# Performance work log

Hardware: AMD Instinct MI355X
Metric: run time of the kernel (lower is better)

Reference implementation:

```python
import jax, jax.numpy as jnp
import numpy as np

N = 131072   # total inner-graph nodes (G * n)
G = 2048     # number of inner graphs = nodes of outer graph fg
n = 64       # nodes per inner graph (contiguous blocks)
E = 1048576  # inner edges
EF = 32768   # outer (fg) edges
D = 128      # emb_dim == hidden_dim
K = 8        # SortPooling k
VOCAB = 150


def setup_inputs() -> dict:
    key = jax.random.key(0)
    ks = jax.random.split(key, 32)
    p = lambda k, shape: (jax.random.normal(k, shape, jnp.float32) * 0.1)
    inp = {
        'h': jax.random.randint(ks[0], (N,), 0, VOCAB),
        'g_src': jax.random.randint(ks[1], (E,), 0, N),
        'g_dst': jax.random.randint(ks[2], (E,), 0, N),
        'fg_src': jax.random.randint(ks[3], (EF,), 0, G),
        'fg_dst': jax.random.randint(ks[4], (EF,), 0, G),
        'token_emb': p(ks[5], (VOCAB, D)),
        # GATConv 1 (D -> D, 1 head): fc weight (in,out), attn vectors, output bias
        'W1': p(ks[6], (D, D)), 'al1': p(ks[7], (D,)), 'ar1': p(ks[8], (D,)), 'b1': p(ks[9], (D,)),
        # GATConv 2
        'W2': p(ks[10], (D, D)), 'al2': p(ks[11], (D,)), 'ar2': p(ks[12], (D,)), 'b2': p(ks[13], (D,)),
        # GATConv 3 (K*D -> D) over fg
        'W3': p(ks[14], (K * D, D)), 'al3': p(ks[15], (D,)), 'ar3': p(ks[16], (D,)), 'b3': p(ks[17], (D,)),
        # linear_forward
        'Wf': p(ks[18], (D, D)), 'bf': p(ks[19], (D,)),
        # linear
        'Wl': p(ks[20], (D, D)), 'bl': p(ks[21], (D,)),
        # linear1
        'Wl1': p(ks[22], (D, D)), 'bl1': p(ks[23], (D,)),
        # clasifier
        'Wc': p(ks[24], (D, 2)), 'bc': p(ks[25], (2,)),
    }
    return inp


def gat_conv(src, dst, num_nodes, x, W, al, ar, b):
    """DGL GATConv, num_heads=1, allow_zero_in_degree=True, no activation."""
    f = x @ W                                   # [N, D] projected features
    el = f @ al                                 # [N] left attention logits
    er = f @ ar                                 # [N] right attention logits
    e = jax.nn.leaky_relu(el[src] + er[dst], 0.2)   # [E] per-edge score
    m = jax.ops.segment_max(e, dst, num_segments=num_nodes)
    a = jnp.exp(e - m[dst])
    s = jax.ops.segment_sum(a, dst, num_segments=num_nodes)
    alpha = a / s[dst]                          # edge softmax over incoming edges
    out = jax.ops.segment_sum(alpha[:, None] * f[src], dst, num_segments=num_nodes)
    return out + b                              # zero-in-degree nodes -> bias only


def sort_pooling(x, num_graphs, nodes_per_graph, k):
    """DGL SortPooling: sort each node's feature ascending, rank nodes by last
    channel descending, take top-k, concat -> [G, k*D]."""
    d = x.shape[-1]
    x = jnp.sort(x.reshape(num_graphs, nodes_per_graph, d), axis=-1)
    idx = jnp.argsort(-x[:, :, -1], axis=1)[:, :k]          # [G, k]
    topk = jnp.take_along_axis(x, idx[:, :, None], axis=1)  # [G, k, D]
    return topk.reshape(num_graphs, k * d)


def reference(h, g_src, g_dst, fg_src, fg_dst, token_emb,
              W1, al1, ar1, b1, W2, al2, ar2, b2, W3, al3, ar3, b3,
              Wf, bf, Wl, bl, Wl1, bl1, Wc, bc):
    x = jax.nn.relu(token_emb[h])                                   # [N, D]
    x = jax.nn.relu(gat_conv(g_src, g_dst, N, x, W1, al1, ar1, b1))
    x = jax.nn.relu(gat_conv(g_src, g_dst, N, x, W2, al2, ar2, b2))
    x = jax.nn.relu(x @ Wf + bf)                                    # linear_forward
    x = sort_pooling(x, G, n, K)                                    # [G, K*D]
    x = jax.nn.relu(gat_conv(fg_src, fg_dst, G, x, W3, al3, ar3, b3))
    x = jax.nn.relu(x @ Wl + bl)                                    # dropout = eval identity
    x = jax.nn.relu(x @ Wl1 + bl1)
    x = x @ Wc + bc
    return x.reshape(-1, 2)
```

## Files before the change

kernel.cpp:

```cpp
#include <hip/hip_runtime.h>
#include <math.h>

#define NN   131072
#define GG   2048
#define NPG  64
#define EE   1048576
#define EFN  32768
#define DD   128
#define KK   8

typedef unsigned short bfu;
typedef short bf16x8 __attribute__((ext_vector_type(8)));
typedef float f32x4 __attribute__((ext_vector_type(4)));

static __device__ __forceinline__ bfu f2b(float f) {
  unsigned u = __float_as_uint(f);
  u += 0x7FFFu + ((u >> 16) & 1u);
  return (bfu)(u >> 16);
}
static __device__ __forceinline__ float b2f(bfu b) {
  return __uint_as_float(((unsigned)b) << 16);
}

__global__ void fill_f32_kernel(float* __restrict__ p, float v, int nElems) {
  int i = blockIdx.x * 256 + threadIdx.x;
  if (i < nElems) p[i] = v;
}

__global__ void zero_int_kernel(int* __restrict__ p, int nElems) {
  int i = blockIdx.x * 256 + threadIdx.x;
  if (i < nElems) p[i] = 0;
}

__global__ void init_softmax_kernel(float* __restrict__ mx, float* __restrict__ sm, int nElems) {
  int i = blockIdx.x * 256 + threadIdx.x;
  if (i < nElems) { mx[i] = -INFINITY; sm[i] = 0.f; }
}

__global__ void embed_relu_kernel(const float* __restrict__ temb,
                                  const int* __restrict__ h,
                                  float* __restrict__ x, int total) {
  int i = blockIdx.x * 256 + threadIdx.x;
  if (i >= total) return;
  int node = i >> 7, d = i & 127;
  x[i] = fmaxf(temb[h[node] * DD + d], 0.f);
}

template <int KD, int ROWS>
__global__ __launch_bounds__(128) void gemm_kernel(
    const float* __restrict__ A, const float* __restrict__ W,
    const float* __restrict__ bias, float* __restrict__ out,
    int relu_flag) {
  __shared__ float As[ROWS * KD];
  const int row0 = blockIdx.x * ROWS;
  const int tid = threadIdx.x;
  for (int i = tid; i < ROWS * KD; i += 128) As[i] = A[(size_t)row0 * KD + i];
  __syncthreads();
  float acc[ROWS];
#pragma unroll
  for (int r = 0; r < ROWS; r++) acc[r] = 0.f;
  for (int k = 0; k < KD; k++) {
    float w = W[k * 128 + tid];
#pragma unroll
    for (int r = 0; r < ROWS; r++) acc[r] += As[r * KD + k] * w;
  }
  float b = bias ? bias[tid] : 0.f;
#pragma unroll
  for (int r = 0; r < ROWS; r++) {
    float v = acc[r] + b;
    if (relu_flag) v = fmaxf(v, 0.f);
    out[(size_t)(row0 + r) * 128 + tid] = v;
  }
}

__global__ __launch_bounds__(256) void gemm1024_kernel(
    const float* __restrict__ A, const float* __restrict__ W,
    float* __restrict__ out) {
  __shared__ float As[8 * 1024];
  __shared__ float red[8][256];
  const int t = threadIdx.x;
  const int row0 = blockIdx.x * 8;
  for (int idx = t; idx < 8 * 256; idx += 256) {
    int r = idx >> 8, c4 = (idx & 255) << 2;
    *(float4*)&As[r * 1024 + c4] = *(const float4*)(A + (size_t)(row0 + r) * 1024 + c4);
  }
  __syncthreads();
  const int col = t & 127, kh = t >> 7;
  const int k0 = kh * 512;
  float acc[8];
#pragma unroll
  for (int r = 0; r < 8; r++) acc[r] = 0.f;
  for (int k = k0; k < k0 + 512; k += 4) {
    float w0 = W[(size_t)(k + 0) * 128 + col];
    float w1 = W[(size_t)(k + 1) * 128 + col];
    float w2 = W[(size_t)(k + 2) * 128 + col];
    float w3 = W[(size_t)(k + 3) * 128 + col];
#pragma unroll
    for (int r = 0; r < 8; r++) {
      float4 a = *(const float4*)&As[r * 1024 + k];
      acc[r] += a.x * w0 + a.y * w1 + a.z * w2 + a.w * w3;
    }
  }
#pragma unroll
  for (int r = 0; r < 8; r++) red[r][t] = acc[r];
  __syncthreads();
  for (int idx = t; idx < 1024; idx += 256) {
    int r = idx >> 7, c = idx & 127;
    out[(size_t)(row0 + r) * 128 + c] = red[r][c] + red[r][128 + c];
  }
}

__global__ void pack_w_kernel(const float* __restrict__ W,
                              bfu* __restrict__ hi, bfu* __restrict__ lo) {
  int i = blockIdx.x * 256 + threadIdx.x;
  if (i >= 16384) return;
  int k = i >> 7, n = i & 127;
  float w = W[i];
  bfu h = f2b(w);
  bfu l = f2b(w - b2f(h));
  int kk = k >> 5, k5 = k & 31, quad = k5 >> 3, j = k5 & 7;
  int tt = n >> 4, m16 = n & 15;
  int pos = ((((kk * 8 + tt) * 4 + quad) * 16) + m16) * 8 + j;
  hi[pos] = h;
  lo[pos] = l;
}

template <int SRC_MODE, int EPI>
__global__ __launch_bounds__(256) void mfma_gemm(
    const float* A, const float* __restrict__ temb,
    const int* __restrict__ hidx,
    const bfu* __restrict__ WfHi, const bfu* __restrict__ WfLo,
    const float* __restrict__ bias, void* out,
    const float* __restrict__ al, const float* __restrict__ ar,
    float* __restrict__ el, float* __restrict__ er,
    float* __restrict__ keyb) {
  const int t = threadIdx.x;
  const int lane = t & 63, wv_ = t >> 6;
  const int m16 = lane & 15, quad = lane >> 4;
  const int rowbase = blockIdx.x * 128 + wv_ * 32;
  const float* arow0 = (SRC_MODE == 1) ? (temb + (size_t)hidx[rowbase + m16] * 128)
                                       : (A + (size_t)(rowbase + m16) * 128);
  const float* arow1 = (SRC_MODE == 1) ? (temb + (size_t)hidx[rowbase + 16 + m16] * 128)
                                       : (A + (size_t)(rowbase + 16 + m16) * 128);
  f32x4 acc[2][8];
#pragma unroll
  for (int rg = 0; rg < 2; rg++)
#pragma unroll
    for (int i = 0; i < 8; i++) acc[rg][i] = (f32x4){0.f, 0.f, 0.f, 0.f};
#pragma unroll
  for (int kk = 0; kk < 4; kk++) {
    int k0 = kk * 32 + quad * 8;
    float av0[8], av1[8];
    *(float4*)&av0[0] = *(const float4*)(arow0 + k0);
    *(float4*)&av0[4] = *(const float4*)(arow0 + k0 + 4);
    *(float4*)&av1[0] = *(const float4*)(arow1 + k0);
    *(float4*)&av1[4] = *(const float4*)(arow1 + k0 + 4);
    if (SRC_MODE == 1) {
#pragma unroll
      for (int i = 0; i < 8; i++) {
        av0[i] = fmaxf(av0[i], 0.f);
        av1[i] = fmaxf(av1[i], 0.f);
      }
    }
    bf16x8 ahi0, alo0, ahi1, alo1;
#pragma unroll
    for (int i = 0; i < 8; i++) {
      bfu h0 = f2b(av0[i]);
      alo0[i] = (short)f2b(av0[i] - b2f(h0));
      ahi0[i] = (short)h0;
      bfu h1 = f2b(av1[i]);
      alo1[i] = (short)f2b(av1[i] - b2f(h1));
      ahi1[i] = (short)h1;
    }
#pragma unroll
    for (int tt = 0; tt < 8; tt++) {
      int pos = ((((kk * 8 + tt) * 4 + quad) * 16) + m16) * 8;
      bf16x8 bhi = *(const bf16x8*)&WfHi[pos];
      bf16x8 blo = *(const bf16x8*)&WfLo[pos];
      acc[0][tt] = __builtin_amdgcn_mfma_f32_16x16x32_bf16(ahi0, bhi, acc[0][tt], 0, 0, 0);
      acc[0][tt] = __builtin_amdgcn_mfma_f32_16x16x32_bf16(ahi0, blo, acc[0][tt], 0, 0, 0);
      acc[0][tt] = __builtin_amdgcn_mfma_f32_16x16x32_bf16(alo0, bhi, acc[0][tt], 0, 0, 0);
      acc[1][tt] = __builtin_amdgcn_mfma_f32_16x16x32_bf16(ahi1, bhi, acc[1][tt], 0, 0, 0);
      acc[1][tt] = __builtin_amdgcn_mfma_f32_16x16x32_bf16(ahi1, blo, acc[1][tt], 0, 0, 0);
      acc[1][tt] = __builtin_amdgcn_mfma_f32_16x16x32_bf16(alo1, bhi, acc[1][tt], 0, 0, 0);
    }
  }
#pragma unroll
  for (int rg = 0; rg < 2; rg++) {
    const int rb = rowbase + rg * 16;
    if (EPI == 1) {
      float pl[4] = {0.f, 0.f, 0.f, 0.f}, pr[4] = {0.f, 0.f, 0.f, 0.f};
#pragma unroll
      for (int tt = 0; tt < 8; tt++) {
        int col = tt * 16 + m16;
        float alv = al[col], arv = ar[col];
#pragma unroll
        for (int r = 0; r < 4; r++) {
          float v = acc[rg][tt][r];
          ((bfu*)out)[(size_t)(rb + quad * 4 + r) * 128 + col] = f2b(v);
          pl[r] += v * alv;
          pr[r] += v * arv;
        }
      }
#pragma unroll
      for (int r = 0; r < 4; r++) {
        float a0 = pl[r], a1 = pr[r];
#pragma unroll
        for (int off = 1; off < 16; off <<= 1) {
          a0 += __shfl_xor(a0, off);
          a1 += __shfl_xor(a1, off);
        }
        if (m16 == 0) {
          el[rb + quad * 4 + r] = a0;
          er[rb + quad * 4 + r] = a1;
        }
      }
    } else {
      float pm[4] = {-INFINITY, -INFINITY, -INFINITY, -INFINITY};
#pragma unroll
      for (int tt = 0; tt < 8; tt++) {
        int col = tt * 16 + m16;
        float bv = bias[col];
#pragma unroll
        for (int r = 0; r < 4; r++) {
          float v = fmaxf(acc[rg][tt][r] + bv, 0.f);
          ((float*)out)[(size_t)(rb + quad * 4 + r) * 128 + col] = v;
          pm[r] = fmaxf(pm[r], v);
        }
      }
#pragma unroll
      for (int r = 0; r < 4; r++) {
        float a0 = pm[r];
#pragma unroll
        for (int off = 1; off < 16; off <<= 1) a0 = fmaxf(a0, __shfl_xor(a0, off));
        if (m16 == 0) keyb[rb + quad * 4 + r] = a0;
      }
    }
  }
}

__global__ __launch_bounds__(64) void attn_logits_kernel(
    const float* __restrict__ f, const float* __restrict__ al,
    const float* __restrict__ ar, float* __restrict__ el,
    float* __restrict__ er) {
  int node = blockIdx.x, lane = threadIdx.x;
  float v1 = f[(size_t)node * 128 + lane];
  float v2 = f[(size_t)node * 128 + 64 + lane];
  float sl = v1 * al[lane] + v2 * al[64 + lane];
  float sr = v1 * ar[lane] + v2 * ar[64 + lane];
#pragma unroll
  for (int off = 32; off; off >>= 1) {
    sl += __shfl_down(sl, off);
    sr += __shfl_down(sr, off);
  }
  if (lane == 0) { el[node] = sl; er[node] = sr; }
}

__global__ void hist_rank_kernel(const int* __restrict__ dst, int* __restrict__ cnt,
                                 int* __restrict__ rank, int nE) {
  int e = blockIdx.x * 256 + threadIdx.x;
  if (e < nE) rank[e] = atomicAdd(&cnt[dst[e]], 1);
}

__global__ __launch_bounds__(256) void scan_block_kernel(
    const int* __restrict__ cnt, int* __restrict__ excl, int* __restrict__ part) {
  __shared__ int s[256];
  int blk = blockIdx.x, tid = threadIdx.x;
  int base = blk * 1024 + tid * 4;
  int a0 = cnt[base], a1 = cnt[base + 1], a2 = cnt[base + 2], a3 = cnt[base + 3];
  int tsum = a0 + a1 + a2 + a3;
  s[tid] = tsum; __syncthreads();
  for (int off = 1; off < 256; off <<= 1) {
    int v = (tid >= off) ? s[tid - off] : 0;
    __syncthreads();
    s[tid] += v;
    __syncthreads();
  }
  int texcl = s[tid] - tsum;
  excl[base]     = texcl;
  excl[base + 1] = texcl + a0;
  excl[base + 2] = texcl + a0 + a1;
  excl[base + 3] = texcl + a0 + a1 + a2;
  if (tid == 255) part[blk] = s[255];
}

__global__ __launch_bounds__(128) void scan_part_kernel(int* __restrict__ part) {
  __shared__ int s[128];
  int tid = threadIdx.x;
  int orig = part[tid];
  s[tid] = orig; __syncthreads();
  for (int off = 1; off < 128; off <<= 1) {
    int v = (tid >= off) ? s[tid - off] : 0;
    __syncthreads();
    s[tid] += v;
    __syncthreads();
  }
  part[tid] = s[tid] - orig;
}

__global__ void scan_add_kernel(int* __restrict__ row_ptr, const int* __restrict__ part,
                                int n, int total) {
  int i = blockIdx.x * 256 + threadIdx.x;
  if (i < n) row_ptr[i] += part[i >> 10];
  if (i == 0) row_ptr[n] = total;
}

__global__ __launch_bounds__(256) void scan2048_kernel(const int* __restrict__ cnt,
                                                       int* __restrict__ rp, int total) {
  __shared__ int s[256];
  int t = threadIdx.x;
  int base = t * 8;
  int v[8];
  int tsum = 0;
#pragma unroll
  for (int i = 0; i < 8; i++) { v[i] = cnt[base + i]; tsum += v[i]; }
  s[t] = tsum; __syncthreads();
  for (int off = 1; off < 256; off <<= 1) {
    int x = (t >= off) ? s[t - off] : 0;
    __syncthreads();
    s[t] += x;
    __syncthreads();
  }
  int excl = s[t] - tsum;
#pragma unroll
  for (int i = 0; i < 8; i++) { rp[base + i] = excl; excl += v[i]; }
  if (t == 255) rp[2048] = total;
}

__global__ void scatter2_kernel(const int* __restrict__ dst, const int* __restrict__ src,
                                const int* __restrict__ row_ptr, const int* __restrict__ rank,
                                int* __restrict__ adj_src, int nE) {
  int e = blockIdx.x * 256 + threadIdx.x;
  if (e >= nE) return;
  adj_src[row_ptr[dst[e]] + rank[e]] = src[e];
}

__global__ __launch_bounds__(256) void gat_aggregate_csr_kernel(
    const bfu* __restrict__ F, const float* __restrict__ el,
    const float* __restrict__ er, const int* __restrict__ row_ptr,
    const int* __restrict__ adj_src,
    const float* __restrict__ bias, float* __restrict__ outX) {
  const int t = threadIdx.x;
  const int l = t & 31;
  const int gb = t & 32;
  const int d = blockIdx.x * 8 + (t >> 5);
  const int c0 = l * 4;
  int beg = row_ptr[d];
  int n = row_ptr[d + 1] - beg;
  float4 bv = *(const float4*)&bias[c0];
  if (n == 0) {
    float4 o;
    o.x = fmaxf(bv.x, 0.f); o.y = fmaxf(bv.y, 0.f);
    o.z = fmaxf(bv.z, 0.f); o.w = fmaxf(bv.w, 0.f);
    *(float4*)&outX[(size_t)d * 128 + c0] = o;
    return;
  }
  float er_d = er[d];
  float4 acc = make_float4(0.f, 0.f, 0.f, 0.f);
  if (n <= 32) {
    int sv = 0; float sc = -INFINITY;
    if (l < n) {
      sv = adj_src[beg + l];
      float v = el[sv] + er_d;
      sc = v > 0.f ? v : 0.2f * v;
    }
    float m = sc;
#pragma unroll
    for (int off = 16; off; off >>= 1) m = fmaxf(m, __shfl_xor(m, off));
    float ex = (l < n) ? expf(sc - m) : 0.f;
    float s = ex;
#pragma unroll
    for (int off = 16; off; off >>= 1) s += __shfl_xor(s, off);
    float wt = ex / s;
    for (int j = 0; j < n; j += 4) {
      int   s0 = __shfl(sv, gb + j);
      float w0 = __shfl(wt, gb + j);
      int   j1 = (j + 1 < n) ? j + 1 : j;
      int   s1 = __shfl(sv, gb + j1); float w1 = (j + 1 < n) ? __shfl(wt, gb + j1) : 0.f;
      int   j2 = (j + 2 < n) ? j + 2 : j;
      int   s2 = __shfl(sv, gb + j2); float w2 = (j + 2 < n) ? __shfl(wt, gb + j2) : 0.f;
      int   j3 = (j + 3 < n) ? j + 3 : j;
      int   s3 = __shfl(sv, gb + j3); float w3 = (j + 3 < n) ? __shfl(wt, gb + j3) : 0.f;
      ushort4 f0 = *(const ushort4*)&F[(size_t)s0 * 128 + c0];
      ushort4 f1 = *(const ushort4*)&F[(size_t)s1 * 128 + c0];
      ushort4 f2 = *(const ushort4*)&F[(size_t)s2 * 128 + c0];
      ushort4 f3 = *(const ushort4*)&F[(size_t)s3 * 128 + c0];
      acc.x += w0 * b2f(f0.x) + w1 * b2f(f1.x) + w2 * b2f(f2.x) + w3 * b2f(f3.x);
      acc.y += w0 * b2f(f0.y) + w1 * b2f(f1.y) + w2 * b2f(f2.y) + w3 * b2f(f3.y);
      acc.z += w0 * b2f(f0.z) + w1 * b2f(f1.z) + w2 * b2f(f2.z) + w3 * b2f(f3.z);
      acc.w += w0 * b2f(f0.w) + w1 * b2f(f1.w) + w2 * b2f(f2.w) + w3 * b2f(f3.w);
    }
  } else {
    float lm = -INFINITY;
    for (int e = l; e < n; e += 32) {
      int sv = adj_src[beg + e];
      float v = el[sv] + er_d;
      v = v > 0.f ? v : 0.2f * v;
      lm = fmaxf(lm, v);
    }
#pragma unroll
    for (int off = 16; off; off >>= 1) lm = fmaxf(lm, __shfl_xor(lm, off));
    float ls = 0.f;
    for (int e = l; e < n; e += 32) {
      int sv = adj_src[beg + e];
      float v = el[sv] + er_d;
      v = v > 0.f ? v : 0.2f * v;
      ls += expf(v - lm);
    }
#pragma unroll
    for (int off = 16; off; off >>= 1) ls += __shfl_xor(ls, off);
    for (int base = 0; base < n; base += 32) {
      int e = base + l;
      int sv = 0; float wt = 0.f;
      if (e < n) {
        sv = adj_src[beg + e];
        float v = el[sv] + er_d;
        v = v > 0.f ? v : 0.2f * v;
        wt = expf(v - lm) / ls;
      }
      int cnt = min(32, n - base);
      for (int j = 0; j < cnt; ++j) {
        int s0 = __shfl(sv, gb + j);
        float w0 = __shfl(wt, gb + j);
        ushort4 f0 = *(const ushort4*)&F[(size_t)s0 * 128 + c0];
        acc.x += w0 * b2f(f0.x);
        acc.y += w0 * b2f(f0.y);
        acc.z += w0 * b2f(f0.z);
        acc.w += w0 * b2f(f0.w);
      }
    }
  }
  float4 o;
  o.x = fmaxf(acc.x + bv.x, 0.f);
  o.y = fmaxf(acc.y + bv.y, 0.f);
  o.z = fmaxf(acc.z + bv.z, 0.f);
  o.w = fmaxf(acc.w + bv.w, 0.f);
  *(float4*)&outX[(size_t)d * 128 + c0] = o;
}

__global__ __launch_bounds__(256) void gat_aggregate_outer_kernel(
    const float* __restrict__ F, const float* __restrict__ el,
    const float* __restrict__ er, const int* __restrict__ row_ptr,
    const int* __restrict__ adj_src,
    const float* __restrict__ bias, float* __restrict__ outG) {
  const int t = threadIdx.x;
  const int l = t & 31;
  const int gb = t & 32;
  const int d = blockIdx.x * 8 + (t >> 5);
  const int c0 = l * 4;
  int beg = row_ptr[d];
  int n = row_ptr[d + 1] - beg;
  float4 bv = *(const float4*)&bias[c0];
  if (n == 0) {
    float4 o;
    o.x = fmaxf(bv.x, 0.f); o.y = fmaxf(bv.y, 0.f);
    o.z = fmaxf(bv.z, 0.f); o.w = fmaxf(bv.w, 0.f);
    *(float4*)&outG[(size_t)d * 128 + c0] = o;
    return;
  }
  float er_d = er[d];
  float4 acc = make_float4(0.f, 0.f, 0.f, 0.f);
  if (n <= 32) {
    int sv = 0; float sc = -INFINITY;
    if (l < n) {
      sv = adj_src[beg + l];
      float v = el[sv] + er_d;
      sc = v > 0.f ? v : 0.2f * v;
    }
    float m = sc;
#pragma unroll
    for (int off = 16; off; off >>= 1) m = fmaxf(m, __shfl_xor(m, off));
    float ex = (l < n) ? expf(sc - m) : 0.f;
    float s = ex;
#pragma unroll
    for (int off = 16; off; off >>= 1) s += __shfl_xor(s, off);
    float wt = ex / s;
    for (int j = 0; j < n; ++j) {
      int   s0 = __shfl(sv, gb + j);
      float w0 = __shfl(wt, gb + j);
      float4 f0 = *(const float4*)&F[(size_t)s0 * 128 + c0];
      acc.x += w0 * f0.x; acc.y += w0 * f0.y;
      acc.z += w0 * f0.z; acc.w += w0 * f0.w;
    }
  } else {
    float lm = -INFINITY;
    for (int e = l; e < n; e += 32) {
      int sv = adj_src[beg + e];
      float v = el[sv] + er_d;
      v = v > 0.f ? v : 0.2f * v;
      lm = fmaxf(lm, v);
    }
#pragma unroll
    for (int off = 16; off; off >>= 1) lm = fmaxf(lm, __shfl_xor(lm, off));
    float ls = 0.f;
    for (int e = l; e < n; e += 32) {
      int sv = adj_src[beg + e];
      float v = el[sv] + er_d;
      v = v > 0.f ? v : 0.2f * v;
      ls += expf(v - lm);
    }
#pragma unroll
    for (int off = 16; off; off >>= 1) ls += __shfl_xor(ls, off);
    for (int base = 0; base < n; base += 32) {
      int e = base + l;
      int sv = 0; float wt = 0.f;
      if (e < n) {
        sv = adj_src[beg + e];
        float v = el[sv] + er_d;
        v = v > 0.f ? v : 0.2f * v;
        wt = expf(v - lm) / ls;
      }
      int cnt = min(32, n - base);
      for (int j = 0; j < cnt; ++j) {
        int s0 = __shfl(sv, gb + j);
        float w0 = __shfl(wt, gb + j);
        float4 f0 = *(const float4*)&F[(size_t)s0 * 128 + c0];
        acc.x += w0 * f0.x; acc.y += w0 * f0.y;
        acc.z += w0 * f0.z; acc.w += w0 * f0.w;
      }
    }
  }
  float4 o;
  o.x = fmaxf(acc.x + bv.x, 0.f);
  o.y = fmaxf(acc.y + bv.y, 0.f);
  o.z = fmaxf(acc.z + bv.z, 0.f);
  o.w = fmaxf(acc.w + bv.w, 0.f);
  *(float4*)&outG[(size_t)d * 128 + c0] = o;
}

static __device__ __forceinline__ void atomicMaxF(float* addr, float v) {
  int iv = __float_as_int(v);
  if (iv >= 0) atomicMax((int*)addr, iv);
  else atomicMin((unsigned int*)addr, (unsigned int)iv);
}

static __device__ __forceinline__ float edge_score(const float* el, const float* er,
                                                   int sv, int dv) {
  float v = el[sv] + er[dv];
  return v > 0.f ? v : 0.2f * v;
}

__global__ void edge_max_kernel(const float* __restrict__ el,
                                const float* __restrict__ er,
                                const int* __restrict__ src,
                                const int* __restrict__ dst,
                                float* __restrict__ m, int nE) {
  int e = blockIdx.x * 256 + threadIdx.x;
  if (e >= nE) return;
  atomicMaxF(&m[dst[e]], edge_score(el, er, src[e], dst[e]));
}

__global__ void edge_expsum_kernel(const float* __restrict__ el,
                                   const float* __restrict__ er,
                                   const float* __restrict__ m,
                                   const int* __restrict__ src,
                                   const int* __restrict__ dst,
                                   float* __restrict__ s, int nE) {
  int e = blockIdx.x * 256 + threadIdx.x;
  if (e >= nE) return;
  int d = dst[e];
  atomicAdd(&s[d], expf(edge_score(el, er, src[e], d) - m[d]));
}

__global__ __launch_bounds__(128) void edge_aggregate_kernel(
    const float* __restrict__ f, const float* __restrict__ el,
    const float* __restrict__ er, const float* __restrict__ m,
    const float* __restrict__ s, const int* __restrict__ src,
    const int* __restrict__ dst, float* __restrict__ out, int nE) {
  int e = blockIdx.x;
  int d = threadIdx.x;
  int sv = src[e], dv = dst[e];
  float alpha = expf(edge_score(el, er, sv, dv) - m[dv]) / s[dv];
  atomicAdd(&out[(size_t)dv * 128 + d], alpha * f[(size_t)sv * 128 + d]);
}

__global__ void bias_relu_kernel(float* __restrict__ x,
                                 const float* __restrict__ b, int total) {
  int i = blockIdx.x * 256 + threadIdx.x;
  if (i >= total) return;
  x[i] = fmaxf(x[i] + b[i & 127], 0.f);
}

__global__ __launch_bounds__(64) void row_max_kernel(const float* __restrict__ x,
                                                     float* __restrict__ key) {
  int node = blockIdx.x, lane = threadIdx.x;
  float v = fmaxf(x[(size_t)node * 128 + lane], x[(size_t)node * 128 + 64 + lane]);
#pragma unroll
  for (int off = 32; off; off >>= 1) v = fmaxf(v, __shfl_down(v, off));
  if (lane == 0) key[node] = v;
}

__global__ __launch_bounds__(64) void select_topk_kernel(
    const float* __restrict__ key, int* __restrict__ sel) {
  __shared__ float keys[NPG];
  int g = blockIdx.x, t = threadIdx.x;
  keys[t] = key[(size_t)g * NPG + t];
  __syncthreads();
  float myk = keys[t];
  int rank = 0;
  for (int j = 0; j < NPG; ++j) {
    float kj = keys[j];
    rank += (kj > myk) || (kj == myk && j < t);
  }
  if (rank < KK) sel[g * KK + rank] = t;
}

__global__ __launch_bounds__(128) void sort_rows_kernel(
    const float* __restrict__ x, const int* __restrict__ sel,
    float* __restrict__ xp) {
  __shared__ float v[128];
  int b = blockIdx.x;
  int t = threadIdx.x;
  int g = b >> 3, r = b & 7;
  int node = sel[b];
  v[t] = x[(size_t)(g * NPG + node) * 128 + t];
  __syncthreads();
  for (int k = 2; k <= 128; k <<= 1) {
    for (int j = k >> 1; j > 0; j >>= 1) {
      int ixj = t ^ j;
      if (ixj > t) {
        float a = v[t], bb = v[ixj];
        bool asc = ((t & k) == 0);
        if (asc ? (a > bb) : (a < bb)) { v[t] = bb; v[ixj] = a; }
      }
      __syncthreads();
    }
  }
  xp[(size_t)g * (KK * 128) + r * 128 + t] = v[t];
}

__global__ __launch_bounds__(128) void mlp_tail_kernel(
    const float* __restrict__ g3, const float* __restrict__ Wl,
    const float* __restrict__ bl, const float* __restrict__ Wl1,
    const float* __restrict__ bl1, const float* __restrict__ Wc,
    const float* __restrict__ bc, float* __restrict__ out) {
  __shared__ float buf[128];
  __shared__ float r0[128], r1[128];
  int g = blockIdx.x, t = threadIdx.x;
  buf[t] = g3[(size_t)g * 128 + t];
  __syncthreads();
  float a = 0.f;
  for (int k = 0; k < 128; k++) a += buf[k] * Wl[k * 128 + t];
  float t1 = fmaxf(a + bl[t], 0.f);
  __syncthreads();
  buf[t] = t1;
  __syncthreads();
  a = 0.f;
  for (int k = 0; k < 128; k++) a += buf[k] * Wl1[k * 128 + t];
  float t2 = fmaxf(a + bl1[t], 0.f);
  r0[t] = t2 * Wc[t * 2 + 0];
  r1[t] = t2 * Wc[t * 2 + 1];
  __syncthreads();
  for (int off = 64; off; off >>= 1) {
    if (t < off) { r0[t] += r0[t + off]; r1[t] += r1[t + off]; }
    __syncthreads();
  }
  if (t == 0) {
    out[g * 2 + 0] = r0[0] + bc[0];
    out[g * 2 + 1] = r1[0] + bc[1];
  }
}

extern "C" void kernel_launch(void* const* d_in, const int* in_sizes, int n_in,
                              void* d_out, int out_size, void* d_ws, size_t ws_size,
                              hipStream_t stream) {
  const size_t BASE_FLOATS = (size_t)NN * DD * 2 + (size_t)NN * 4;
  const size_t CSR_INTS = (size_t)(NN + 1) + NN + EE + 128;
  if (ws_size < BASE_FLOATS * sizeof(float)) {
    hipMemsetAsync(d_out, 0, (size_t)out_size * sizeof(float), stream);
    return;
  }
  const bool use_csr = ws_size >= BASE_FLOATS * sizeof(float) + CSR_INTS * sizeof(int);

  const int* h      = (const int*)d_in[0];
  const int* g_src  = (const int*)d_in[1];
  const int* g_dst  = (const int*)d_in[2];
  const int* fg_src = (const int*)d_in[3];
  const int* fg_dst = (const int*)d_in[4];
  const float* temb = (const float*)d_in[5];
  const float* W1 = (const float*)d_in[6];
  const float* al1 = (const float*)d_in[7];
  const float* ar1 = (const float*)d_in[8];
  const float* b1 = (const float*)d_in[9];
  const float* W2 = (const float*)d_in[10];
  const float* al2 = (const float*)d_in[11];
  const float* ar2 = (const float*)d_in[12];
  const float* b2 = (const float*)d_in[13];
  const float* W3 = (const float*)d_in[14];
  const float* al3 = (const float*)d_in[15];
  const float* ar3 = (const float*)d_in[16];
  const float* b3 = (const float*)d_in[17];
  const float* Wf = (const float*)d_in[18];
  const float* bfv = (const float*)d_in[19];
  const float* Wl = (const float*)d_in[20];
  const float* bl = (const float*)d_in[21];
  const float* Wl1 = (const float*)d_in[22];
  const float* bl1 = (const float*)d_in[23];
  const float* Wc = (const float*)d_in[24];
  const float* bc = (const float*)d_in[25];
  float* out = (float*)d_out;

  float* ws = (float*)d_ws;
  float* X  = ws;
  float* F  = X + (size_t)NN * DD;
  float* el = F + (size_t)NN * DD;
  float* er = el + NN;
  float* mx = er + NN;
  float* sm = mx + NN;
  int* row_ptr = (int*)(sm + NN);
  int* cursor  = row_ptr + NN + 1;
  int* adj_src = cursor + NN;
  int* part    = adj_src + EE;
  int* rankb = (int*)X;
  bfu* w1h = (bfu*)mx;
  bfu* w1l = w1h + 16384;
  bfu* w2h = w1l + 16384;
  bfu* w2l = w2h + 16384;
  bfu* wfh = w2l + 16384;
  bfu* wfl = wfh + 16384;
  int* ocnt  = (int*)X;
  int* orp   = ocnt + 2048;
  int* orank = orp + 2080;
  int* oadj  = orank + EFN;
  float* xp   = F;
  float* f3   = F + 2097152;
  float* g3   = f3 + (size_t)GG * DD;
  float* t1   = g3 + (size_t)GG * DD;
  float* t2   = t1 + (size_t)GG * DD;
  float* keyb = t2 + (size_t)GG * DD;
  int*   sel  = (int*)(keyb + NN);

  const int totalND = NN * DD;

  if (use_csr) {
    bfu* Fb = (bfu*)F;
    zero_int_kernel<<<NN / 256, 256, 0, stream>>>(cursor, NN);
    hist_rank_kernel<<<EE / 256, 256, 0, stream>>>(g_dst, cursor, rankb, EE);
    scan_block_kernel<<<NN / 1024, 256, 0, stream>>>(cursor, row_ptr, part);
    scan_part_kernel<<<1, 128, 0, stream>>>(part);
    scan_add_kernel<<<(NN + 255) / 256, 256, 0, stream>>>(row_ptr, part, NN, EE);
    scatter2_kernel<<<EE / 256, 256, 0, stream>>>(g_dst, g_src, row_ptr, rankb, adj_src, EE);

    pack_w_kernel<<<64, 256, 0, stream>>>(W1, w1h, w1l);
    pack_w_kernel<<<64, 256, 0, stream>>>(W2, w2h, w2l);
    pack_w_kernel<<<64, 256, 0, stream>>>(Wf, wfh, wfl);

    mfma_gemm<1, 1><<<NN / 128, 256, 0, stream>>>(
        nullptr, temb, h, w1h, w1l, nullptr, Fb, al1, ar1, el, er, nullptr);
    gat_aggregate_csr_kernel<<<NN / 8, 256, 0, stream>>>(Fb, el, er, row_ptr, adj_src, b1, X);

    mfma_gemm<0, 1><<<NN / 128, 256, 0, stream>>>(
        X, nullptr, nullptr, w2h, w2l, nullptr, Fb, al2, ar2, el, er, nullptr);
    gat_aggregate_csr_kernel<<<NN / 8, 256, 0, stream>>>(Fb, el, er, row_ptr, adj_src, b2, X);

    mfma_gemm<0, 2><<<NN / 128, 256, 0, stream>>>(
        X, nullptr, nullptr, wfh, wfl, bfv, X, nullptr, nullptr, nullptr, nullptr, keyb);

    select_topk_kernel<<<GG, 64, 0, stream>>>(keyb, sel);
    sort_rows_kernel<<<GG * KK, 128, 0, stream>>>(X, sel, xp);

    gemm1024_kernel<<<GG / 8, 256, 0, stream>>>(xp, W3, f3);
    attn_logits_kernel<<<GG, 64, 0, stream>>>(f3, al3, ar3, el, er);
    zero_int_kernel<<<GG / 256, 256, 0, stream>>>(ocnt, GG);
    hist_rank_kernel<<<EFN / 256, 256, 0, stream>>>(fg_dst, ocnt, orank, EFN);
    scan2048_kernel<<<1, 256, 0, stream>>>(ocnt, orp, EFN);
    scatter2_kernel<<<EFN / 256, 256, 0, stream>>>(fg_dst, fg_src, orp, orank, oadj, EFN);
    gat_aggregate_outer_kernel<<<GG / 8, 256, 0, stream>>>(f3, el, er, orp, oadj, b3, g3);

    mlp_tail_kernel<<<GG, 128, 0, stream>>>(g3, Wl, bl, Wl1, bl1, Wc, bc, out);
  } else {
    embed_relu_kernel<<<totalND / 256, 256, 0, stream>>>(temb, h, X, totalND);
    auto gat_inner = [&](const float* W, const float* al, const float* ar, const float* bb) {
      gemm_kernel<DD, 8><<<NN / 8, 128, 0, stream>>>(X, W, nullptr, F, 0);
      attn_logits_kernel<<<NN, 64, 0, stream>>>(F, al, ar, el, er);
      init_softmax_kernel<<<(NN + 255) / 256, 256, 0, stream>>>(mx, sm, NN);
      fill_f32_kernel<<<totalND / 256, 256, 0, stream>>>(X, 0.f, totalND);
      edge_max_kernel<<<(EE + 255) / 256, 256, 0, stream>>>(el, er, g_src, g_dst, mx, EE);
      edge_expsum_kernel<<<(EE + 255) / 256, 256, 0, stream>>>(el, er, mx, g_src, g_dst, sm, EE);
      edge_aggregate_kernel<<<EE, 128, 0, stream>>>(F, el, er, mx, sm, g_src, g_dst, X, EE);
      bias_relu_kernel<<<totalND / 256, 256, 0, stream>>>(X, bb, totalND);
    };
    gat_inner(W1, al1, ar1, b1);
    gat_inner(W2, al2, ar2, b2);
    gemm_kernel<DD, 8><<<NN / 8, 128, 0, stream>>>(X, Wf, bfv, X, 1);
    row_max_kernel<<<NN, 64, 0, stream>>>(X, keyb);

    select_topk_kernel<<<GG, 64, 0, stream>>>(keyb, sel);
    sort_rows_kernel<<<GG * KK, 128, 0, stream>>>(X, sel, xp);

    gemm1024_kernel<<<GG / 8, 256, 0, stream>>>(xp, W3, f3);
    attn_logits_kernel<<<GG, 64, 0, stream>>>(f3, al3, ar3, el, er);
    init_softmax_kernel<<<(GG + 255) / 256, 256, 0, stream>>>(mx, sm, GG);
    fill_f32_kernel<<<(GG * DD + 255) / 256, 256, 0, stream>>>(g3, 0.f, GG * DD);
    edge_max_kernel<<<(EFN + 255) / 256, 256, 0, stream>>>(el, er, fg_src, fg_dst, mx, EFN);
    edge_expsum_kernel<<<(EFN + 255) / 256, 256, 0, stream>>>(el, er, mx, fg_src, fg_dst, sm, EFN);
    edge_aggregate_kernel<<<EFN, 128, 0, stream>>>(f3, el, er, mx, sm, fg_src, fg_dst, g3, EFN);
    bias_relu_kernel<<<(GG * DD + 255) / 256, 256, 0, stream>>>(g3, b3, GG * DD);
    mlp_tail_kernel<<<GG, 128, 0, stream>>>(g3, Wl, bl, Wl1, bl1, Wc, bc, out);
  }
}
```

Before: 473.6 us.

## Switch inner GAT activations and MFMA split to fp16, store X as half

Replaces the bf16 hi/lo split with an fp16 hi/lo split for weights and projected features. Aggregation outputs and the linear_forward output are now stored as fp16 instead of fp32, halving activation traffic. The two subsequent GEMMs read them directly through a new source mode, skipping the A-lo correction MFMA and the fp32-to-split conversion. The risk is fp16 range and precision loss on activations, plus a changed numeric path feeding sort pooling's ranking and ties.

```diff
diff --git a/kernel.cpp b/kernel.cpp
--- a/kernel.cpp
+++ b/kernel.cpp
@@ -10,7 +10,7 @@
 #define KK   8
 
 typedef unsigned short bfu;
-typedef short bf16x8 __attribute__((ext_vector_type(8)));
+typedef _Float16 f16x8 __attribute__((ext_vector_type(8)));
 typedef float f32x4 __attribute__((ext_vector_type(4)));
 
 static __device__ __forceinline__ bfu f2b(float f) {
@@ -20,6 +20,18 @@
 }
 static __device__ __forceinline__ float b2f(bfu b) {
   return __uint_as_float(((unsigned)b) << 16);
+}
+
+static __device__ __forceinline__ bfu f2h(float f) {
+  _Float16 h = (_Float16)f;
+  bfu u;
+  __builtin_memcpy(&u, &h, 2);
+  return u;
+}
+static __device__ __forceinline__ float h2f(bfu b) {
+  _Float16 h;
+  __builtin_memcpy(&h, &b, 2);
+  return (float)h;
 }
 
 __global__ void fill_f32_kernel(float* __restrict__ p, float v, int nElems) {
@@ -116,8 +128,8 @@
   if (i >= 16384) return;
   int k = i >> 7, n = i & 127;
   float w = W[i];
-  bfu h = f2b(w);
-  bfu l = f2b(w - b2f(h));
+  bfu h = f2h(w);
+  bfu l = f2h(w - h2f(h));
   int kk = k >> 5, k5 = k & 31, quad = k5 >> 3, j = k5 & 7;
   int tt = n >> 4, m16 = n & 15;
   int pos = ((((kk * 8 + tt) * 4 + quad) * 16) + m16) * 8 + j;
@@ -138,10 +150,20 @@
   const int lane = t & 63, wv_ = t >> 6;
   const int m16 = lane & 15, quad = lane >> 4;
   const int rowbase = blockIdx.x * 128 + wv_ * 32;
-  const float* arow0 = (SRC_MODE == 1) ? (temb + (size_t)hidx[rowbase + m16] * 128)
-                                       : (A + (size_t)(rowbase + m16) * 128);
-  const float* arow1 = (SRC_MODE == 1) ? (temb + (size_t)hidx[rowbase + 16 + m16] * 128)
-                                       : (A + (size_t)(rowbase + 16 + m16) * 128);
+  const float* arow0 = nullptr;
+  const float* arow1 = nullptr;
+  const bfu* brow0 = nullptr;
+  const bfu* brow1 = nullptr;
+  if constexpr (SRC_MODE == 1) {
+    arow0 = temb + (size_t)hidx[rowbase + m16] * 128;
+    arow1 = temb + (size_t)hidx[rowbase + 16 + m16] * 128;
+  } else if constexpr (SRC_MODE == 0) {
+    arow0 = A + (size_t)(rowbase + m16) * 128;
+    arow1 = A + (size_t)(rowbase + 16 + m16) * 128;
+  } else {
+    brow0 = (const bfu*)A + (size_t)(rowbase + m16) * 128;
+    brow1 = (const bfu*)A + (size_t)(rowbase + 16 + m16) * 128;
+  }
   f32x4 acc[2][8];
 #pragma unroll
   for (int rg = 0; rg < 2; rg++)
@@ -150,45 +172,52 @@
 #pragma unroll
   for (int kk = 0; kk < 4; kk++) {
     int k0 = kk * 32 + quad * 8;
-    float av0[8], av1[8];
-    *(float4*)&av0[0] = *(const float4*)(arow0 + k0);
-    *(float4*)&av0[4] = *(const float4*)(arow0 + k0 + 4);
-    *(float4*)&av1[0] = *(const float4*)(arow1 + k0);
-    *(float4*)&av1[4] = *(const float4*)(arow1 + k0 + 4);
-    if (SRC_MODE == 1) {
+    f16x8 ahi0, alo0, ahi1, alo1;
+    if constexpr (SRC_MODE == 2) {
+      ahi0 = *(const f16x8*)(brow0 + k0);
+      ahi1 = *(const f16x8*)(brow1 + k0);
+    } else {
+      float av0[8], av1[8];
+      *(float4*)&av0[0] = *(const float4*)(arow0 + k0);
+      *(float4*)&av0[4] = *(const float4*)(arow0 + k0 + 4);
+      *(float4*)&av1[0] = *(const float4*)(arow1 + k0);
+      *(float4*)&av1[4] = *(const float4*)(arow1 + k0 + 4);
+      if (SRC_MODE == 1) {
+#pragma unroll
+        for (int i = 0; i < 8; i++) {
+          av0[i] = fmaxf(av0[i], 0.f);
+          av1[i] = fmaxf(av1[i], 0.f);
+        }
+      }
 #pragma unroll
       for (int i = 0; i < 8; i++) {
-        av0[i] = fmaxf(av0[i], 0.f);
-        av1[i] = fmaxf(av1[i], 0.f);
-      }
-    }
-    bf16x8 ahi0, alo0, ahi1, alo1;
-#pragma unroll
-    for (int i = 0; i < 8; i++) {
-      bfu h0 = f2b(av0[i]);
-      alo0[i] = (short)f2b(av0[i] - b2f(h0));
-      ahi0[i] = (short)h0;
-      bfu h1 = f2b(av1[i]);
-      alo1[i] = (short)f2b(av1[i] - b2f(h1));
-      ahi1[i] = (short)h1;
+        _Float16 h0 = (_Float16)av0[i];
+        ahi0[i] = h0;
+        alo0[i] = (_Float16)(av0[i] - (float)h0);
+        _Float16 h1 = (_Float16)av1[i];
+        ahi1[i] = h1;
+        alo1[i] = (_Float16)(av1[i] - (float)h1);
+      }
     }
 #pragma unroll
     for (int tt = 0; tt < 8; tt++) {
       int pos = ((((kk * 8 + tt) * 4 + quad) * 16) + m16) * 8;
-      bf16x8 bhi = *(const bf16x8*)&WfHi[pos];
-      bf16x8 blo = *(const bf16x8*)&WfLo[pos];
-      acc[0][tt] = __builtin_amdgcn_mfma_f32_16x16x32_bf16(ahi0, bhi, acc[0][tt], 0, 0, 0);
-      acc[0][tt] = __builtin_amdgcn_mfma_f32_16x16x32_bf16(ahi0, blo, acc[0][tt], 0, 0, 0);
-      acc[0][tt] = __builtin_amdgcn_mfma_f32_16x16x32_bf16(alo0, bhi, acc[0][tt], 0, 0, 0);
-      acc[1][tt] = __builtin_amdgcn_mfma_f32_16x16x32_bf16(ahi1, bhi, acc[1][tt], 0, 0, 0);
-      acc[1][tt] = __builtin_amdgcn_mfma_f32_16x16x32_bf16(ahi1, blo, acc[1][tt], 0, 0, 0);
-      acc[1][tt] = __builtin_amdgcn_mfma_f32_16x16x32_bf16(alo1, bhi, acc[1][tt], 0, 0, 0);
+      f16x8 bhi = *(const f16x8*)&WfHi[pos];
+      f16x8 blo = *(const f16x8*)&WfLo[pos];
+      acc[0][tt] = __builtin_amdgcn_mfma_f32_16x16x32_f16(ahi0, bhi, acc[0][tt], 0, 0, 0);
+      acc[0][tt] = __builtin_amdgcn_mfma_f32_16x16x32_f16(ahi0, blo, acc[0][tt], 0, 0, 0);
+      if constexpr (SRC_MODE != 2)
+        acc[0][tt] = __builtin_amdgcn_mfma_f32_16x16x32_f16(alo0, bhi, acc[0][tt], 0, 0, 0);
+      acc[1][tt] = __builtin_amdgcn_mfma_f32_16x16x32_f16(ahi1, bhi, acc[1][tt], 0, 0, 0);
+      acc[1][tt] = __builtin_amdgcn_mfma_f32_16x16x32_f16(ahi1, blo, acc[1][tt], 0, 0, 0);
+      if constexpr (SRC_MODE != 2)
+        acc[1][tt] = __builtin_amdgcn_mfma_f32_16x16x32_f16(alo1, bhi, acc[1][tt], 0, 0, 0);
     }
   }
 #pragma unroll
   for (int rg = 0; rg < 2; rg++) {
     const int rb = rowbase + rg * 16;
-    if (EPI == 1) {
+    if constexpr (EPI == 1) {
       float pl[4] = {0.f, 0.f, 0.f, 0.f}, pr[4] = {0.f, 0.f, 0.f, 0.f};
 #pragma unroll
       for (int tt = 0; tt < 8; tt++) {
@@ -197,7 +226,7 @@
 #pragma unroll
         for (int r = 0; r < 4; r++) {
           float v = acc[rg][tt][r];
-          ((bfu*)out)[(size_t)(rb + quad * 4 + r) * 128 + col] = f2b(v);
+          ((bfu*)out)[(size_t)(rb + quad * 4 + r) * 128 + col] = f2h(v);
           pl[r] += v * alv;
           pr[r] += v * arv;
         }
@@ -224,7 +253,7 @@
 #pragma unroll
         for (int r = 0; r < 4; r++) {
           float v = fmaxf(acc[rg][tt][r] + bv, 0.f);
-          ((float*)out)[(size_t)(rb + quad * 4 + r) * 128 + col] = v;
+          ((bfu*)out)[(size_t)(rb + quad * 4 + r) * 128 + col] = f2h(v);
           pm[r] = fmaxf(pm[r], v);
         }
       }
@@ -339,7 +368,7 @@
     const bfu* __restrict__ F, const float* __restrict__ el,
     const float* __restrict__ er, const int* __restrict__ row_ptr,
     const int* __restrict__ adj_src,
-    const float* __restrict__ bias, float* __restrict__ outX) {
+    const float* __restrict__ bias, bfu* __restrict__ outX) {
   const int t = threadIdx.x;
   const int l = t & 31;
   const int gb = t & 32;
@@ -349,10 +378,10 @@
   int n = row_ptr[d + 1] - beg;
   float4 bv = *(const float4*)&bias[c0];
   if (n == 0) {
-    float4 o;
-    o.x = fmaxf(bv.x, 0.f); o.y = fmaxf(bv.y, 0.f);
-    o.z = fmaxf(bv.z, 0.f); o.w = fmaxf(bv.w, 0.f);
-    *(float4*)&outX[(size_t)d * 128 + c0] = o;
+    ushort4 o;
+    o.x = f2h(fmaxf(bv.x, 0.f)); o.y = f2h(fmaxf(bv.y, 0.f));
+    o.z = f2h(fmaxf(bv.z, 0.f)); o.w = f2h(fmaxf(bv.w, 0.f));
+    *(ushort4*)&outX[(size_t)d * 128 + c0] = o;
     return;
   }
   float er_d = er[d];
@@ -385,10 +414,10 @@
       ushort4 f1 = *(const ushort4*)&F[(size_t)s1 * 128 + c0];
       ushort4 f2 = *(const ushort4*)&F[(size_t)s2 * 128 + c0];
       ushort4 f3 = *(const ushort4*)&F[(size_t)s3 * 128 + c0];
-      acc.x += w0 * b2f(f0.x) + w1 * b2f(f1.x) + w2 * b2f(f2.x) + w3 * b2f(f3.x);
-      acc.y += w0 * b2f(f0.y) + w1 * b2f(f1.y) + w2 * b2f(f2.y) + w3 * b2f(f3.y);
-      acc.z += w0 * b2f(f0.z) + w1 * b2f(f1.z) + w2 * b2f(f2.z) + w3 * b2f(f3.z);
-      acc.w += w0 * b2f(f0.w) + w1 * b2f(f1.w) + w2 * b2f(f2.w) + w3 * b2f(f3.w);
+      acc.x += w0 * h2f(f0.x) + w1 * h2f(f1.x) + w2 * h2f(f2.x) + w3 * h2f(f3.x);
+      acc.y += w0 * h2f(f0.y) + w1 * h2f(f1.y) + w2 * h2f(f2.y) + w3 * h2f(f3.y);
+      acc.z += w0 * h2f(f0.z) + w1 * h2f(f1.z) + w2 * h2f(f2.z) + w3 * h2f(f3.z);
+      acc.w += w0 * h2f(f0.w) + w1 * h2f(f1.w) + w2 * h2f(f2.w) + w3 * h2f(f3.w);
     }
   } else {
     float lm = -INFINITY;
@@ -423,19 +452,19 @@
         int s0 = __shfl(sv, gb + j);
         float w0 = __shfl(wt, gb + j);
         ushort4 f0 = *(const ushort4*)&F[(size_t)s0 * 128 + c0];
-        acc.x += w0 * b2f(f0.x);
-        acc.y += w0 * b2f(f0.y);
-        acc.z += w0 * b2f(f0.z);
-        acc.w += w0 * b2f(f0.w);
-      }
-    }
-  }
-  float4 o;
-  o.x = fmaxf(acc.x + bv.x, 0.f);
-  o.y = fmaxf(acc.y + bv.y, 0.f);
-  o.z = fmaxf(acc.z + bv.z, 0.f);
-  o.w = fmaxf(acc.w + bv.w, 0.f);
-  *(float4*)&outX[(size_t)d * 128 + c0] = o;
+        acc.x += w0 * h2f(f0.x);
+        acc.y += w0 * h2f(f0.y);
+        acc.z += w0 * h2f(f0.z);
+        acc.w += w0 * h2f(f0.w);
+      }
+    }
+  }
+  ushort4 o;
+  o.x = f2h(fmaxf(acc.x + bv.x, 0.f));
+  o.y = f2h(fmaxf(acc.y + bv.y, 0.f));
+  o.z = f2h(fmaxf(acc.z + bv.z, 0.f));
+  o.w = f2h(fmaxf(acc.w + bv.w, 0.f));
+  *(ushort4*)&outX[(size_t)d * 128 + c0] = o;
 }
 
 __global__ __launch_bounds__(256) void gat_aggregate_outer_kernel(
@@ -605,15 +634,17 @@
   if (rank < KK) sel[g * KK + rank] = t;
 }
 
+template <int HF>
 __global__ __launch_bounds__(128) void sort_rows_kernel(
-    const float* __restrict__ x, const int* __restrict__ sel,
+    const void* __restrict__ xin, const int* __restrict__ sel,
     float* __restrict__ xp) {
   __shared__ float v[128];
   int b = blockIdx.x;
   int t = threadIdx.x;
   int g = b >> 3, r = b & 7;
   int node = sel[b];
-  v[t] = x[(size_t)(g * NPG + node) * 128 + t];
+  if (HF) v[t] = h2f(((const bfu*)xin)[(size_t)(g * NPG + node) * 128 + t]);
+  else    v[t] = ((const float*)xin)[(size_t)(g * NPG + node) * 128 + t];
   __syncthreads();
   for (int k = 2; k <= 128; k <<= 1) {
     for (int j = k >> 1; j > 0; j >>= 1) {
@@ -734,6 +765,7 @@
 
   if (use_csr) {
     bfu* Fb = (bfu*)F;
+    bfu* Xb = (bfu*)X;
     zero_int_kernel<<<NN / 256, 256, 0, stream>>>(cursor, NN);
     hist_rank_kernel<<<EE / 256, 256, 0, stream>>>(g_dst, cursor, rankb, EE);
     scan_block_kernel<<<NN / 1024, 256, 0, stream>>>(cursor, row_ptr, part);
@@ -747,17 +779,17 @@
 
     mfma_gemm<1, 1><<<NN / 128, 256, 0, stream>>>(
         nullptr, temb, h, w1h, w1l, nullptr, Fb, al1, ar1, el, er, nullptr);
-    gat_aggregate_csr_kernel<<<NN / 8, 256, 0, stream>>>(Fb, el, er, row_ptr, adj_src, b1, X);
-
-    mfma_gemm<0, 1><<<NN / 128, 256, 0, stream>>>(
-        X, nullptr, nullptr, w2h, w2l, nullptr, Fb, al2, ar2, el, er, nullptr);
-    gat_aggregate_csr_kernel<<<NN / 8, 256, 0, stream>>>(Fb, el, er, row_ptr, adj_src, b2, X);
-
-    mfma_gemm<0, 2><<<NN / 128, 256, 0, stream>>>(
-        X, nullptr, nullptr, wfh, wfl, bfv, X, nullptr, nullptr, nullptr, nullptr, keyb);
+    gat_aggregate_csr_kernel<<<NN / 8, 256, 0, stream>>>(Fb, el, er, row_ptr, adj_src, b1, Xb);
+
+    mfma_gemm<2, 1><<<NN / 128, 256, 0, stream>>>(
+        (const float*)X, nullptr, nullptr, w2h, w2l, nullptr, Fb, al2, ar2, el, er, nullptr);
+    gat_aggregate_csr_kernel<<<NN / 8, 256, 0, stream>>>(Fb, el, er, row_ptr, adj_src, b2, Xb);
+
+    mfma_gemm<2, 2><<<NN / 128, 256, 0, stream>>>(
+        (const float*)X, nullptr, nullptr, wfh, wfl, bfv, Xb, nullptr, nullptr, nullptr, nullptr, keyb);
 
     select_topk_kernel<<<GG, 64, 0, stream>>>(keyb, sel);
-    sort_rows_kernel<<<GG * KK, 128, 0, stream>>>(X, sel, xp);
+    sort_rows_kernel<1><<<GG * KK, 128, 0, stream>>>(Xb, sel, xp);
 
     gemm1024_kernel<<<GG / 8, 256, 0, stream>>>(xp, W3, f3);
     attn_logits_kernel<<<GG, 64, 0, stream>>>(f3, al3, ar3, el, er);
@@ -786,7 +818,7 @@
     row_max_kernel<<<NN, 64, 0, stream>>>(X, keyb);
 
     select_topk_kernel<<<GG, 64, 0, stream>>>(keyb, sel);
-    sort_rows_kernel<<<GG * KK, 128, 0, stream>>>(X, sel, xp);
+    sort_rows_kernel<0><<<GG * KK, 128, 0, stream>>>(X, sel, xp);
 
     gemm1024_kernel<<<GG / 8, 256, 0, stream>>>(xp, W3, f3);
     attn_logits_kernel<<<GG, 64, 0, stream>>>(f3, al3, ar3, el, er);
```

Result: faster. 461.8 us (-2.5%).
